# Kernel optimization log

Measured on AMD Instinct MI355X. Metric: run time of the kernel, lower is better.

## Reference

```python
import jax, jax.numpy as jnp
import numpy as np

B, T, C = 8, 512, 2048          # batch streams, qlen, hidden_size
H, Z = 32, 64                   # num_heads, head_size; A = H*Z = attention_hidden_size
A = H * Z
TMX, TDX = 32, 64               # TIME_MIX_EXTRA_DIM, TIME_DECAY_EXTRA_DIM
EPS = 1e-5 * 8.0**2             # ln_x eps = 1e-5 * head_size_divisor**2


def setup_inputs() -> dict:
    key = jax.random.key(0)
    ks = jax.random.split(key, 24)
    def rn(i, shape, scale=1.0):
        return jax.random.normal(ks[i], shape, jnp.float32) * scale
    inv_c = 1.0 / np.sqrt(C)
    return {
        "hidden_states": rn(0, (B * T, C)),
        "positions": jnp.zeros((B * T,), jnp.int32),
        "input_kv_state": jnp.zeros((B, H, Z, Z), jnp.float32),
        "input_shift_state": rn(1, (B, C)),
        "time_maa_x": rn(2, (1, 1, C), 0.1),
        "time_maa_w": rn(3, (1, 1, C), 0.1),
        "time_maa_k": rn(4, (1, 1, C), 0.1),
        "time_maa_v": rn(5, (1, 1, C), 0.1),
        "time_maa_r": rn(6, (1, 1, C), 0.1),
        "time_maa_g": rn(7, (1, 1, C), 0.1),
        "time_maa_w1": rn(8, (C, TMX * 5), inv_c),
        "time_maa_w2": rn(9, (5, TMX, C), 1.0 / np.sqrt(TMX)),
        "time_decay": rn(10, (1, 1, A), 0.5),
        "time_decay_w1": rn(11, (C, TDX), inv_c),
        "time_decay_w2": rn(12, (TDX, A), 0.01),
        "time_faaaa": rn(13, (H, Z), 0.1),
        "W_r": rn(14, (C, A), inv_c),
        "W_k": rn(15, (C, A), inv_c),
        "W_v": rn(16, (C, A), inv_c),
        "W_g": rn(17, (C, A), inv_c),
        "W_o": rn(18, (A, C), inv_c),
        "ln_w": 1.0 + rn(19, (C,), 0.1),
        "ln_b": rn(20, (C,), 0.1),
    }


def _rwkv6_forward(hidden_states, positions, input_kv_state, input_shift_state,
                   time_maa_x, time_maa_w, time_maa_k, time_maa_v, time_maa_r,
                   time_maa_g, time_maa_w1, time_maa_w2, time_decay,
                   time_decay_w1, time_decay_w2, time_faaaa,
                   W_r, W_k, W_v, W_g, W_o, ln_w, ln_b):
    x = hidden_states.reshape(B, T, C)
    pos0_is_zero = positions.reshape(B, T)[:, 0] == 0
    reset = jnp.where(pos0_is_zero, -100.0, 0.0)  # [B]
    # kill shift state for fresh sequences (matches * exp(-100))
    shift = input_shift_state * jnp.exp(reset)[:, None]  # [B, C]

    # token-shift mixing (shift state broadcast over T, as in source)
    xx = shift[:, None, :] - x  # [B, T, C]
    xxx = x + xx * time_maa_x
    mix = jnp.tanh(xxx @ time_maa_w1).reshape(B, T, 5, TMX)
    mix = jnp.einsum('btfe,fec->fbtc', mix, time_maa_w2)  # [5, B, T, C]
    mw, mk, mv, mr, mg = mix

    td_in = x + xx * (time_maa_w + mw)
    kx = x + xx * (time_maa_k + mk)
    vx = x + xx * (time_maa_v + mv)
    rx = x + xx * (time_maa_r + mr)
    gx = x + xx * (time_maa_g + mg)

    r = rx @ W_r
    k = kx @ W_k
    v = vx @ W_v
    g = jax.nn.silu(gx @ W_g)  # [B, T, A]

    w = time_decay + jnp.tanh(td_in @ time_decay_w1) @ time_decay_w2
    w = -jnp.exp(w.astype(jnp.float32))  # log-decay, [B, T, A]

    # split heads -> [T, B, H, Z] for scan
    def to_tbhz(a):
        return a.reshape(B, T, H, Z).transpose(1, 0, 2, 3)
    r_s, k_s, v_s, w_s = to_tbhz(r), to_tbhz(k), to_tbhz(v), to_tbhz(w)
    # zero out carried state at t=0 for fresh sequences
    w_s = w_s.at[0].add(reset[:, None, None])

    u = time_faaaa  # [H, Z]

    def step(S, rkvw):
        # S: [B, H, K, V] (key-dim x value-dim state)
        r_t, k_t, v_t, w_t = rkvw  # each [B, H, Z]
        kv = k_t[..., :, None] * v_t[..., None, :]  # [B, H, K, V]
        o = jnp.einsum('bhk,bhkv->bhv', r_t, S + u[None, :, :, None] * kv)
        S = jnp.exp(w_t)[..., None] * S + kv
        return S, o

    S_out, o = jax.lax.scan(step, input_kv_state, (r_s, k_s, v_s, w_s))
    xo = o.transpose(1, 0, 2, 3).reshape(B * T, C)  # [B*T, C]

    # GroupNorm over heads (num_groups = H)
    xg = xo.reshape(B * T, H, Z)
    mu = xg.mean(-1, keepdims=True)
    var = xg.var(-1, keepdims=True)
    xn = ((xg - mu) * jax.lax.rsqrt(var + EPS)).reshape(B * T, C) * ln_w + ln_b

    out = (xn.reshape(B, T, C) * g) @ W_o  # [B, T, C]
    return out.reshape(B * T, C)


def reference(hidden_states, positions, input_kv_state, input_shift_state,
              time_maa_x, time_maa_w, time_maa_k, time_maa_v, time_maa_r,
              time_maa_g, time_maa_w1, time_maa_w2, time_decay,
              time_decay_w1, time_decay_w2, time_faaaa,
              W_r, W_k, W_v, W_g, W_o, ln_w, ln_b):
    return _rwkv6_forward(hidden_states, positions, input_kv_state,
                          input_shift_state, time_maa_x, time_maa_w,
                          time_maa_k, time_maa_v, time_maa_r, time_maa_g,
                          time_maa_w1, time_maa_w2, time_decay, time_decay_w1,
                          time_decay_w2, time_faaaa, W_r, W_k, W_v, W_g, W_o,
                          ln_w, ln_b)
```

## Files before the change

### kernel.cpp

```cpp
#include <hip/hip_runtime.h>
#include <cmath>

#define NB 8
#define NT 512
#define NC 2048
#define NH 32
#define NZ 64
static constexpr float GN_EPS = 1e-5f * 64.0f;

typedef _Float16 f16;
typedef __attribute__((ext_vector_type(8))) _Float16 f16x8;
typedef __attribute__((ext_vector_type(4))) _Float16 f16x4;
typedef __attribute__((ext_vector_type(4))) float f4;

static __device__ __forceinline__ void gload16(const void* gp, void* lp) {
  __builtin_amdgcn_global_load_lds(
      (const __attribute__((address_space(1))) void*)gp,
      (__attribute__((address_space(3))) void*)lp, 16, 0, 0);
}

__global__ void k_transpose_cast(const float* __restrict__ in, f16* __restrict__ out,
                                 int R, int Cc) {
  __shared__ float tile[32][33];
  int c0 = blockIdx.x * 32, r0 = blockIdx.y * 32;
  int tx = threadIdx.x, ty = threadIdx.y;
#pragma unroll
  for (int i = 0; i < 4; ++i)
    tile[ty + i * 8][tx] = in[(size_t)(r0 + ty + i * 8) * Cc + c0 + tx];
  __syncthreads();
#pragma unroll
  for (int i = 0; i < 4; ++i)
    out[(size_t)(c0 + ty + i * 8) * R + r0 + tx] = (f16)tile[tx][ty + i * 8];
}

__global__ void k_transpose_split(const float* __restrict__ in, f16* __restrict__ ohi,
                                  f16* __restrict__ olo, int R, int Cc) {
  __shared__ float tile[32][33];
  int c0 = blockIdx.x * 32, r0 = blockIdx.y * 32;
  int tx = threadIdx.x, ty = threadIdx.y;
#pragma unroll
  for (int i = 0; i < 4; ++i)
    tile[ty + i * 8][tx] = in[(size_t)(r0 + ty + i * 8) * Cc + c0 + tx];
  __syncthreads();
#pragma unroll
  for (int i = 0; i < 4; ++i) {
    float v = tile[tx][ty + i * 8];
    f16 h = (f16)v;
    size_t o = (size_t)(c0 + ty + i * 8) * R + r0 + tx;
    ohi[o] = h;
    olo[o] = (f16)(v - (float)h);
  }
}

__global__ void k_tsplit_w2(const float* __restrict__ in0, f16* __restrict__ ohi0,
                            f16* __restrict__ olo0) {
  __shared__ float tile[32][33];
  int f = blockIdx.z;
  const float* in = in0 + (size_t)f * 32 * 2048;
  f16* ohi = ohi0 + (size_t)f * 2048 * 32;
  f16* olo = olo0 + (size_t)f * 2048 * 32;
  int c0 = blockIdx.x * 32;
  int tx = threadIdx.x, ty = threadIdx.y;
#pragma unroll
  for (int i = 0; i < 4; ++i)
    tile[ty + i * 8][tx] = in[(size_t)(ty + i * 8) * 2048 + c0 + tx];
  __syncthreads();
#pragma unroll
  for (int i = 0; i < 4; ++i) {
    float v = tile[tx][ty + i * 8];
    f16 h = (f16)v;
    size_t o = (size_t)(c0 + ty + i * 8) * 32 + tx;
    ohi[o] = h;
    olo[o] = (f16)(v - (float)h);
  }
}

__global__ void k_xxx(const float* __restrict__ hs, const float* __restrict__ shift_st,
                      const int* __restrict__ positions, const float* __restrict__ maa_x,
                      float* __restrict__ xxx) {
  int i = blockIdx.x * blockDim.x + threadIdx.x;
  int idx = i * 4;
  int c = idx & (NC - 1);
  int t = idx >> 11;
  int b = t >> 9;
  float er = (positions[b * NT] == 0) ? expf(-100.0f) : 1.0f;
  const float4 x = *(const float4*)(hs + idx);
  const float4 sh = *(const float4*)(shift_st + b * NC + c);
  const float4 mx = *(const float4*)(maa_x + c);
  float4 o;
  o.x = x.x + (sh.x * er - x.x) * mx.x;
  o.y = x.y + (sh.y * er - x.y) * mx.y;
  o.z = x.z + (sh.z * er - x.z) * mx.z;
  o.w = x.w + (sh.w * er - x.w) * mx.w;
  *(float4*)(xxx + idx) = o;
}

static __device__ __forceinline__ void split4(const float4 v, int base, f16x8& hi, f16x8& lo) {
  float x[4] = {v.x, v.y, v.z, v.w};
#pragma unroll
  for (int j = 0; j < 4; ++j) {
    f16 h = (f16)x[j];
    hi[base + j] = h;
    lo[base + j] = (f16)(x[j] - (float)h);
  }
}

__global__ __launch_bounds__(64) void k_mix1_split(const float* __restrict__ A,
                                                   const f16* __restrict__ Bhi,
                                                   const f16* __restrict__ Blo,
                                                   float* __restrict__ out) {
  int m0 = blockIdx.x * 16, n0 = blockIdx.y * 16;
  int lane = threadIdx.x, lr = lane & 15, kq = lane >> 4;
  f4 acc = {0.f, 0.f, 0.f, 0.f};
  const float* ap = A + (size_t)(m0 + lr) * 2048 + kq * 8;
  const f16* bh0 = Bhi + (size_t)(n0 + lr) * 2048 + kq * 8;
  const f16* bl0 = Blo + (size_t)(n0 + lr) * 2048 + kq * 8;
  for (int k0 = 0; k0 < 2048; k0 += 32) {
    f16x8 ah, al;
    split4(*(const float4*)(ap + k0), 0, ah, al);
    split4(*(const float4*)(ap + k0 + 4), 4, ah, al);
    f16x8 bh = *(const f16x8*)(bh0 + k0);
    f16x8 bl = *(const f16x8*)(bl0 + k0);
    acc = __builtin_amdgcn_mfma_f32_16x16x32_f16(ah, bh, acc, 0, 0, 0);
    acc = __builtin_amdgcn_mfma_f32_16x16x32_f16(ah, bl, acc, 0, 0, 0);
    acc = __builtin_amdgcn_mfma_f32_16x16x32_f16(al, bh, acc, 0, 0, 0);
  }
#pragma unroll
  for (int r = 0; r < 4; ++r)
    out[(size_t)(m0 + kq * 4 + r) * 160 + n0 + lr] = tanhf(acc[r]);
}

__global__ __launch_bounds__(64) void k_tmp5_split(const float* __restrict__ mixb,
    const f16* __restrict__ Bhi, const f16* __restrict__ Blo,
    const float* __restrict__ hs, const float* __restrict__ shift_st,
    const int* __restrict__ positions,
    const float* __restrict__ maa_w, const float* __restrict__ maa_k,
    const float* __restrict__ maa_v, const float* __restrict__ maa_r,
    const float* __restrict__ maa_g,
    float* __restrict__ tdin, f16* __restrict__ kx, f16* __restrict__ vx,
    f16* __restrict__ rx, f16* __restrict__ gx) {
  int m0 = blockIdx.x * 16, n0 = blockIdx.y * 16;
  int lane = threadIdx.x, lr = lane & 15, kq = lane >> 4;
  f4 acc[5];
#pragma unroll
  for (int f = 0; f < 5; ++f) acc[f] = (f4){0.f, 0.f, 0.f, 0.f};
  const float* ap = mixb + (size_t)(m0 + lr) * 160 + kq * 8;
#pragma unroll
  for (int f = 0; f < 5; ++f) {
    f16x8 ah, al;
    split4(*(const float4*)(ap + f * 32), 0, ah, al);
    split4(*(const float4*)(ap + f * 32 + 4), 4, ah, al);
    size_t bi = ((size_t)f * 2048 + n0 + lr) * 32 + kq * 8;
    f16x8 bh = *(const f16x8*)(Bhi + bi);
    f16x8 bl = *(const f16x8*)(Blo + bi);
    acc[f] = __builtin_amdgcn_mfma_f32_16x16x32_f16(ah, bh, acc[f], 0, 0, 0);
    acc[f] = __builtin_amdgcn_mfma_f32_16x16x32_f16(ah, bl, acc[f], 0, 0, 0);
    acc[f] = __builtin_amdgcn_mfma_f32_16x16x32_f16(al, bh, acc[f], 0, 0, 0);
  }
  int c = n0 + lr;
  float mw = maa_w[c], mk = maa_k[c], mv = maa_v[c], mr = maa_r[c], mg = maa_g[c];
#pragma unroll
  for (int r = 0; r < 4; ++r) {
    int t = m0 + kq * 4 + r;
    int b = t >> 9;
    float er = (positions[b * NT] == 0) ? expf(-100.0f) : 1.0f;
    float x = hs[(size_t)t * NC + c];
    float xxv = shift_st[b * NC + c] * er - x;
    size_t oi = (size_t)t * NC + c;
    tdin[oi] = x + xxv * (mw + acc[0][r]);
    kx[oi] = (f16)(x + xxv * (mk + acc[1][r]));
    vx[oi] = (f16)(x + xxv * (mv + acc[2][r]));
    rx[oi] = (f16)(x + xxv * (mr + acc[3][r]));
    gx[oi] = (f16)(x + xxv * (mg + acc[4][r]));
  }
}

__global__ __launch_bounds__(64) void k_wd1_split(const float* __restrict__ A,
                                                  const f16* __restrict__ Bhi,
                                                  const f16* __restrict__ Blo,
                                                  float* __restrict__ out) {
  int m0 = blockIdx.x * 16, n0 = blockIdx.y * 16;
  int lane = threadIdx.x, lr = lane & 15, kq = lane >> 4;
  f4 acc = {0.f, 0.f, 0.f, 0.f};
  const float* ap = A + (size_t)(m0 + lr) * 2048 + kq * 8;
  const f16* bh0 = Bhi + (size_t)(n0 + lr) * 2048 + kq * 8;
  const f16* bl0 = Blo + (size_t)(n0 + lr) * 2048 + kq * 8;
  for (int k0 = 0; k0 < 2048; k0 += 32) {
    f16x8 ah, al;
    split4(*(const float4*)(ap + k0), 0, ah, al);
    split4(*(const float4*)(ap + k0 + 4), 4, ah, al);
    f16x8 bh = *(const f16x8*)(bh0 + k0);
    f16x8 bl = *(const f16x8*)(bl0 + k0);
    acc = __builtin_amdgcn_mfma_f32_16x16x32_f16(ah, bh, acc, 0, 0, 0);
    acc = __builtin_amdgcn_mfma_f32_16x16x32_f16(ah, bl, acc, 0, 0, 0);
    acc = __builtin_amdgcn_mfma_f32_16x16x32_f16(al, bh, acc, 0, 0, 0);
  }
#pragma unroll
  for (int r = 0; r < 4; ++r)
    out[(size_t)(m0 + kq * 4 + r) * 64 + n0 + lr] = tanhf(acc[r]);
}

__global__ __launch_bounds__(64) void k_wdecay_split(const float* __restrict__ A,
                                                     const f16* __restrict__ Bhi,
                                                     const f16* __restrict__ Blo,
                                                     const float* __restrict__ time_decay,
                                                     float* __restrict__ wout) {
  int m0 = blockIdx.x * 16, n0 = blockIdx.y * 16;
  int lane = threadIdx.x, lr = lane & 15, kq = lane >> 4;
  f4 acc = {0.f, 0.f, 0.f, 0.f};
#pragma unroll
  for (int kk = 0; kk < 2; ++kk) {
    f16x8 ah, al;
    const float* ap = A + (size_t)(m0 + lr) * 64 + kk * 32 + kq * 8;
    split4(*(const float4*)ap, 0, ah, al);
    split4(*(const float4*)(ap + 4), 4, ah, al);
    size_t bi = (size_t)(n0 + lr) * 64 + kk * 32 + kq * 8;
    f16x8 bh = *(const f16x8*)(Bhi + bi);
    f16x8 bl = *(const f16x8*)(Blo + bi);
    acc = __builtin_amdgcn_mfma_f32_16x16x32_f16(ah, bh, acc, 0, 0, 0);
    acc = __builtin_amdgcn_mfma_f32_16x16x32_f16(ah, bl, acc, 0, 0, 0);
    acc = __builtin_amdgcn_mfma_f32_16x16x32_f16(al, bh, acc, 0, 0, 0);
  }
  int c = n0 + lr;
  float td = time_decay[c];
#pragma unroll
  for (int r = 0; r < 4; ++r) {
    int t = m0 + kq * 4 + r;
    wout[(size_t)t * NC + c] = -expf(td + acc[r]);
  }
}

#define GBM 128
#define GBN 128
#define GBK 64

template <int EPI>
__global__ __launch_bounds__(256) void k_gemm_big(const f16* __restrict__ A,
                                                  const f16* __restrict__ Bt,
                                                  float* __restrict__ Cf,
                                                  f16* __restrict__ Cb, int K) {
  __shared__ __align__(16) f16 As[2][GBM][GBK];
  __shared__ __align__(16) f16 Bs[2][GBN][GBK];
  int nwg = gridDim.x * gridDim.y;
  int wg = blockIdx.y * gridDim.x + blockIdx.x;
  int swz = (wg & 7) * (nwg >> 3) + (wg >> 3);
  int n0 = (swz % gridDim.x) * GBN;
  int m0 = (swz / gridDim.x) * GBM;
  int tid = threadIdx.x;
  int wid = tid >> 6, lane = tid & 63;
  int wr = wid >> 1, wc = wid & 1;
  int lr = lane & 15, kq = lane >> 4;
  int sw = lr & 7;
  int gunit = (lane & 7) ^ (lane >> 3);
  const f16* aL = A + (size_t)(m0 + wid * 32 + (lane >> 3)) * K + gunit * 8;
  const f16* bL = Bt + (size_t)(n0 + wid * 32 + (lane >> 3)) * K + gunit * 8;
  f4 acc[4][4];
#pragma unroll
  for (int m = 0; m < 4; ++m)
#pragma unroll
    for (int n = 0; n < 4; ++n) acc[m][n] = (f4){0.f, 0.f, 0.f, 0.f};

  auto stage = [&](int buf, int t) {
    int k0 = t * GBK;
#pragma unroll
    for (int i = 0; i < 4; ++i) {
      gload16(aL + k0 + (size_t)i * 8 * K, &As[buf][wid * 32 + i * 8][0]);
      gload16(bL + k0 + (size_t)i * 8 * K, &Bs[buf][wid * 32 + i * 8][0]);
    }
  };

  int niter = K / GBK;
  stage(0, 0);
  stage(1, 1);
  for (int it = 0; it < niter; ++it) {
    if (it == niter - 1)
      asm volatile("s_waitcnt vmcnt(0)" ::: "memory");
    else
      asm volatile("s_waitcnt vmcnt(8)" ::: "memory");
    __builtin_amdgcn_sched_barrier(0);
    __builtin_amdgcn_s_barrier();
    int cur = it & 1;
#pragma unroll
    for (int kk = 0; kk < 2; ++kk) {
      f16x8 af[4], bfv[4];
      int un = ((kk * 4 + kq) ^ sw) * 8;
#pragma unroll
      for (int m = 0; m < 4; ++m)
        af[m] = *(const f16x8*)&As[cur][wr * 64 + m * 16 + lr][un];
#pragma unroll
      for (int n = 0; n < 4; ++n)
        bfv[n] = *(const f16x8*)&Bs[cur][wc * 64 + n * 16 + lr][un];
#pragma unroll
      for (int m = 0; m < 4; ++m)
#pragma unroll
        for (int n = 0; n < 4; ++n)
          acc[m][n] = __builtin_amdgcn_mfma_f32_16x16x32_f16(af[m], bfv[n], acc[m][n], 0, 0, 0);
    }
    __builtin_amdgcn_s_barrier();
    if (it + 2 < niter) stage(cur, it + 2);
  }
#pragma unroll
  for (int m = 0; m < 4; ++m) {
    int row0 = m0 + wr * 64 + m * 16 + kq * 4;
#pragma unroll
    for (int n = 0; n < 4; ++n) {
      int col = n0 + wc * 64 + n * 16 + lr;
#pragma unroll
      for (int r = 0; r < 4; ++r) {
        float v = acc[m][n][r];
        size_t oi = (size_t)(row0 + r) * NC + col;
        if (EPI == 0) {
          Cf[oi] = v;
        } else {
          float s = v / (1.0f + expf(-v));
          Cb[oi] = (f16)s;
        }
      }
    }
  }
}

__global__ __launch_bounds__(64) void k_scanB(
    const float* rb, const float* __restrict__ kb,
    const float* __restrict__ vb, const float* __restrict__ wb,
    const float* __restrict__ kvstate, const int* __restrict__ positions,
    const float* __restrict__ faaaa, f16* __restrict__ o,
    float* rtil, float* __restrict__ Ebuf, float* __restrict__ Dbuf) {
  int blk = blockIdx.x;
  int bh = blk >> 3, c = blk & 7;
  int b = bh >> 5, h = bh & 31;
  int zz = threadIdx.x;
  __shared__ __align__(16) float shR[64];
  __shared__ __align__(16) float shE[64];
  __shared__ __align__(16) float shK[64];
  float S[64];
  if (c == 0) {
    const float* S0 = kvstate + (size_t)bh * 4096;
#pragma unroll
    for (int j = 0; j < 64; ++j) S[j] = S0[j * 64 + zz];
  } else {
#pragma unroll
    for (int j = 0; j < 64; ++j) S[j] = 0.f;
  }
  float u = faaaa[h * 64 + zz];
  float reset = (positions[b * NT] == 0) ? -100.0f : 0.0f;
  const size_t base = ((size_t)(b * NT) + c * 64) * NC + h * 64 + zz;
  float vr = rb[base], vk = kb[base], vw = wb[base], vv = vb[base];
  float Pw = 1.0f;
  for (int t = 0; t < 64; ++t) {
    float nr = 0.f, nk = 0.f, nw = 0.f, nv = 0.f;
    if (t + 1 < 64) {
      size_t idx = base + (size_t)(t + 1) * NC;
      nr = rb[idx]; nk = kb[idx]; nw = wb[idx]; nv = vb[idx];
    }
    float ww = vw;
    if (c == 0 && t == 0) ww += reset;
    float ew = expf(ww);
    shR[zz] = vr; shE[zz] = ew; shK[zz] = vk;
    float q = vr * u * vk;
    q += __shfl_xor(q, 1);  q += __shfl_xor(q, 2);  q += __shfl_xor(q, 4);
    q += __shfl_xor(q, 8);  q += __shfl_xor(q, 16); q += __shfl_xor(q, 32);
    __syncthreads();
    if (c > 0) rtil[base + (size_t)t * NC] = vr * Pw;
    Pw *= ew;
    float oacc = vv * q;
#pragma unroll
    for (int k0 = 0; k0 < 64; k0 += 4) {
      f4 r4 = *(const f4*)&shR[k0];
      f4 e4 = *(const f4*)&shE[k0];
      f4 k4 = *(const f4*)&shK[k0];
#pragma unroll
      for (int j = 0; j < 4; ++j) {
        oacc = fmaf(r4[j], S[k0 + j], oacc);
        S[k0 + j] = fmaf(e4[j], S[k0 + j], k4[j] * vv);
      }
    }
    o[base + (size_t)t * NC] = (f16)oacc;
    __syncthreads();
    vr = nr; vk = nk; vw = nw; vv = nv;
  }
  if (c < 7) {
    float* E = Ebuf + ((size_t)bh * 7 + c) * 4096;
#pragma unroll
    for (int j = 0; j < 64; ++j) E[j * 64 + zz] = S[j];
  }
  Dbuf[((size_t)bh * 8 + c) * 64 + zz] = Pw;
}

__global__ __launch_bounds__(256) void k_comb(float* __restrict__ Ebuf,
                                              const float* __restrict__ Dbuf) {
  int bh = blockIdx.x, tid = threadIdx.x;
  int k = tid >> 2, v0 = (tid & 3) * 16;
  float* base = Ebuf + (size_t)bh * 7 * 4096;
  float S[16];
#pragma unroll
  for (int j = 0; j < 16; ++j) S[j] = base[k * 64 + v0 + j];
  for (int c = 2; c <= 7; ++c) {
    float d = Dbuf[((size_t)bh * 8 + (c - 1)) * 64 + k];
    float* slot = base + (size_t)(c - 1) * 4096;
#pragma unroll
    for (int j = 0; j < 16; ++j) {
      S[j] = fmaf(d, S[j], slot[k * 64 + v0 + j]);
      slot[k * 64 + v0 + j] = S[j];
    }
  }
}

__global__ __launch_bounds__(256) void k_fix(const float* __restrict__ rtil,
                                             const float* __restrict__ Ebuf,
                                             f16* __restrict__ o) {
  int blk = blockIdx.x;
  int bh = blk / 7, cm = blk - bh * 7;
  int c = cm + 1;
  int b = bh >> 5, h = bh & 31;
  __shared__ float Rs[64][65];
  __shared__ float Ss[64][65];
  int tid = threadIdx.x;
  const float* rsrc = rtil + ((size_t)(b * NT) + c * 64) * NC + h * NZ;
  const float* ssrc = Ebuf + ((size_t)bh * 7 + cm) * 4096;
#pragma unroll
  for (int q = 0; q < 4; ++q) {
    int li = tid * 4 + q;
    int rr = li >> 4, cc = (li & 15) * 4;
    float4 x = *(const float4*)(rsrc + (size_t)rr * NC + cc);
    Rs[rr][cc] = x.x; Rs[rr][cc + 1] = x.y; Rs[rr][cc + 2] = x.z; Rs[rr][cc + 3] = x.w;
    float4 y = *(const float4*)(ssrc + rr * 64 + cc);
    Ss[rr][cc] = y.x; Ss[rr][cc + 1] = y.y; Ss[rr][cc + 2] = y.z; Ss[rr][cc + 3] = y.w;
  }
  __syncthreads();
  int t = tid >> 2, v0 = (tid & 3) * 16;
  float acc[16];
#pragma unroll
  for (int j = 0; j < 16; ++j) acc[j] = 0.f;
  for (int k = 0; k < 64; ++k) {
    float rv = Rs[t][k];
#pragma unroll
    for (int j = 0; j < 16; ++j) acc[j] = fmaf(rv, Ss[k][v0 + j], acc[j]);
  }
  f16* op = o + ((size_t)(b * NT) + c * 64 + t) * NC + h * NZ + v0;
  f16x8 o0 = *(f16x8*)op, o1 = *(f16x8*)(op + 8);
#pragma unroll
  for (int j = 0; j < 8; ++j) {
    o0[j] = (f16)((float)o0[j] + acc[j]);
    o1[j] = (f16)((float)o1[j] + acc[j + 8]);
  }
  *(f16x8*)op = o0;
  *(f16x8*)(op + 8) = o1;
}

__global__ __launch_bounds__(256) void k_gnorm(const f16* __restrict__ xo, const f16* __restrict__ g,
    const float* __restrict__ ln_w, const float* __restrict__ ln_b, f16* __restrict__ y) {
  int t = blockIdx.x;
  int tid = threadIdx.x;
  int c = tid * 8;
  f16x8 xv8 = *(const f16x8*)(xo + (size_t)t * NC + c);
  float xv[8];
#pragma unroll
  for (int j = 0; j < 8; ++j) xv[j] = (float)xv8[j];
  float s = 0.f, ss = 0.f;
#pragma unroll
  for (int j = 0; j < 8; ++j) { s += xv[j]; ss += xv[j] * xv[j]; }
  s += __shfl_xor(s, 1); ss += __shfl_xor(ss, 1);
  s += __shfl_xor(s, 2); ss += __shfl_xor(ss, 2);
  s += __shfl_xor(s, 4); ss += __shfl_xor(ss, 4);
  float mu = s * (1.0f / 64.0f);
  float var = ss * (1.0f / 64.0f) - mu * mu;
  float rstd = rsqrtf(var + GN_EPS);
  f16x8 gv = *(const f16x8*)(g + (size_t)t * NC + c);
  f16x8 ov;
#pragma unroll
  for (int j = 0; j < 8; ++j) {
    float xn = (xv[j] - mu) * rstd * ln_w[c + j] + ln_b[c + j];
    ov[j] = (f16)(xn * (float)gv[j]);
  }
  *(f16x8*)(y + (size_t)t * NC + c) = ov;
}

extern "C" void kernel_launch(void* const* d_in, const int* in_sizes, int n_in,
                              void* d_out, int out_size, void* d_ws, size_t ws_size,
                              hipStream_t stream) {
  const float* hs = (const float*)d_in[0];
  const int* positions = (const int*)d_in[1];
  const float* kvstate = (const float*)d_in[2];
  const float* shift_st = (const float*)d_in[3];
  const float* maa_x = (const float*)d_in[4];
  const float* maa_w = (const float*)d_in[5];
  const float* maa_k = (const float*)d_in[6];
  const float* maa_v = (const float*)d_in[7];
  const float* maa_r = (const float*)d_in[8];
  const float* maa_g = (const float*)d_in[9];
  const float* maa_w1 = (const float*)d_in[10];
  const float* maa_w2 = (const float*)d_in[11];
  const float* time_decay = (const float*)d_in[12];
  const float* decay_w1 = (const float*)d_in[13];
  const float* decay_w2 = (const float*)d_in[14];
  const float* faaaa = (const float*)d_in[15];
  const float* W_r = (const float*)d_in[16];
  const float* W_k = (const float*)d_in[17];
  const float* W_v = (const float*)d_in[18];
  const float* W_g = (const float*)d_in[19];
  const float* W_o = (const float*)d_in[20];
  const float* ln_w = (const float*)d_in[21];
  const float* ln_b = (const float*)d_in[22];

  char* ws = (char*)d_ws;
  size_t off = 0;
  auto alloc = [&](size_t n) {
    char* p = ws + off;
    off += (n + 255) & ~(size_t)255;
    return p;
  };
  f16* w1t_hi = (f16*)alloc(160ull * 2048 * 2);
  f16* w1t_lo = (f16*)alloc(160ull * 2048 * 2);
  f16* w2t_hi = (f16*)alloc(5ull * 2048 * 32 * 2);
  f16* w2t_lo = (f16*)alloc(5ull * 2048 * 32 * 2);
  f16* dw1t_hi = (f16*)alloc(64ull * 2048 * 2);
  f16* dw1t_lo = (f16*)alloc(64ull * 2048 * 2);
  f16* dw2t_hi = (f16*)alloc(2048ull * 64 * 2);
  f16* dw2t_lo = (f16*)alloc(2048ull * 64 * 2);
  float* mixb = (float*)alloc(4096ull * 160 * 4);
  float* wd1 = (float*)alloc(4096ull * 64 * 4);
  char* R_A = alloc(4096ull * 2048 * 4);
  char* R_B = alloc(4096ull * 2048 * 4);
  char* R_C = alloc(4096ull * 2048 * 4);
  char* R_D = alloc(4096ull * 2048 * 4);
  char* R_E = alloc(4096ull * 2048 * 2);
  char* F12 = alloc(4096ull * 2048 * 4);
  char* F3 = alloc(4096ull * 2048 * 2);
  char* F4 = alloc(4096ull * 2048 * 2);

  float* xxx = (float*)R_A;
  float* tdin = (float*)R_A;
  float* wbuf = (float*)R_A;
  float* rbuf = (float*)R_B;
  float* kbuf = (float*)R_C;
  float* vbuf = (float*)R_D;
  f16* wstage = (f16*)R_E;
  f16* obuf = (f16*)R_E;
  f16* kx = (f16*)F12;
  f16* vx = (f16*)(F12 + 4096ull * 2048 * 2);
  float* Ebuf = (float*)F12;
  float* Dbuf = (float*)(F12 + 29360128);
  f16* rx = (f16*)F3;
  f16* gbuf = (f16*)F3;
  f16* gx = (f16*)F4;
  f16* wt_o = (f16*)F4;

  dim3 tb(32, 8);
  k_transpose_split<<<dim3(5, 64), tb, 0, stream>>>(maa_w1, w1t_hi, w1t_lo, 2048, 160);
  k_tsplit_w2<<<dim3(64, 1, 5), tb, 0, stream>>>(maa_w2, w2t_hi, w2t_lo);
  k_transpose_split<<<dim3(2, 64), tb, 0, stream>>>(decay_w1, dw1t_hi, dw1t_lo, 2048, 64);
  k_transpose_split<<<dim3(64, 2), tb, 0, stream>>>(decay_w2, dw2t_hi, dw2t_lo, 64, 2048);

  k_xxx<<<8192, 256, 0, stream>>>(hs, shift_st, positions, maa_x, xxx);
  k_mix1_split<<<dim3(256, 10), 64, 0, stream>>>(xxx, w1t_hi, w1t_lo, mixb);
  k_tmp5_split<<<dim3(256, 128), 64, 0, stream>>>(mixb, w2t_hi, w2t_lo, hs, shift_st,
      positions, maa_w, maa_k, maa_v, maa_r, maa_g, tdin, kx, vx, rx, gx);
  k_wd1_split<<<dim3(256, 4), 64, 0, stream>>>(tdin, dw1t_hi, dw1t_lo, wd1);
  k_wdecay_split<<<dim3(256, 128), 64, 0, stream>>>(wd1, dw2t_hi, dw2t_lo, time_decay, wbuf);

  dim3 gg(2048 / GBN, 4096 / GBM);
  k_transpose_cast<<<dim3(64, 64), tb, 0, stream>>>(W_r, wstage, 2048, 2048);
  k_gemm_big<0><<<gg, 256, 0, stream>>>(rx, wstage, rbuf, nullptr, 2048);
  k_transpose_cast<<<dim3(64, 64), tb, 0, stream>>>(W_k, wstage, 2048, 2048);
  k_gemm_big<0><<<gg, 256, 0, stream>>>(kx, wstage, kbuf, nullptr, 2048);
  k_transpose_cast<<<dim3(64, 64), tb, 0, stream>>>(W_v, wstage, 2048, 2048);
  k_gemm_big<0><<<gg, 256, 0, stream>>>(vx, wstage, vbuf, nullptr, 2048);
  k_transpose_cast<<<dim3(64, 64), tb, 0, stream>>>(W_g, wstage, 2048, 2048);
  k_gemm_big<2><<<gg, 256, 0, stream>>>(gx, wstage, nullptr, gbuf, 2048);
  k_transpose_cast<<<dim3(64, 64), tb, 0, stream>>>(W_o, wt_o, 2048, 2048);

  k_scanB<<<2048, 64, 0, stream>>>(rbuf, kbuf, vbuf, wbuf, kvstate, positions, faaaa,
                                   obuf, rbuf, Ebuf, Dbuf);
  k_comb<<<256, 256, 0, stream>>>(Ebuf, Dbuf);
  k_fix<<<1792, 256, 0, stream>>>(rbuf, Ebuf, obuf);

  k_gnorm<<<4096, 256, 0, stream>>>(obuf, gbuf, ln_w, ln_b, obuf);
  k_gemm_big<0><<<gg, 256, 0, stream>>>(obuf, wt_o, (float*)d_out, nullptr, 2048);
}
```

Baseline: 639.9 us.

## Double-buffer scan inputs into LDS with async loads in four-step groups

The chunked WKV scan now stages r, k, w and v rows for four timesteps at a time into LDS. It uses global_load_lds with a double buffer and explicit vmcnt waits, replacing per-timestep register prefetch and three barrier-guarded shared arrays. Decay exponentials are computed for all four steps at once, which cuts barriers from two per timestep to two per group. The goal is to hide global-load latency in a latency-bound scan. The cost is more LDS, and correctness depends on hand-written waitcnt logic and on the single-wave block running in lockstep.

After: 640.2 us. No clear change (+0.1%).

```diff
diff --git a/kernel.cpp b/kernel.cpp
--- a/kernel.cpp
+++ b/kernel.cpp
@@ -320,7 +320,7 @@
   }
 }
 
-__global__ __launch_bounds__(64) void k_scanB(
+__global__ __launch_bounds__(64) void k_scanD(
     const float* rb, const float* __restrict__ kb,
     const float* __restrict__ vb, const float* __restrict__ wb,
     const float* __restrict__ kvstate, const int* __restrict__ positions,
@@ -330,9 +330,8 @@
   int bh = blk >> 3, c = blk & 7;
   int b = bh >> 5, h = bh & 31;
   int zz = threadIdx.x;
-  __shared__ __align__(16) float shR[64];
-  __shared__ __align__(16) float shE[64];
-  __shared__ __align__(16) float shK[64];
+  __shared__ __align__(16) float stg[2][4][4][64];
+  __shared__ __align__(16) float shE[4][64];
   float S[64];
   if (c == 0) {
     const float* S0 = kvstate + (size_t)bh * 4096;
@@ -344,40 +343,63 @@
   }
   float u = faaaa[h * 64 + zz];
   float reset = (positions[b * NT] == 0) ? -100.0f : 0.0f;
-  const size_t base = ((size_t)(b * NT) + c * 64) * NC + h * 64 + zz;
-  float vr = rb[base], vk = kb[base], vw = wb[base], vv = vb[base];
+  const int row0 = b * NT + c * 64;
+  const int lrow = zz >> 4, lcol = (zz & 15) * 4;
+
+  auto stage = [&](int buf, int T) {
+    size_t goff = (size_t)(row0 + T + lrow) * NC + h * 64 + lcol;
+    gload16(rb + goff, &stg[buf][0][0][0]);
+    gload16(kb + goff, &stg[buf][1][0][0]);
+    gload16(wb + goff, &stg[buf][2][0][0]);
+    gload16(vb + goff, &stg[buf][3][0][0]);
+  };
+  stage(0, 0);
+  stage(1, 4);
   float Pw = 1.0f;
-  for (int t = 0; t < 64; ++t) {
-    float nr = 0.f, nk = 0.f, nw = 0.f, nv = 0.f;
-    if (t + 1 < 64) {
-      size_t idx = base + (size_t)(t + 1) * NC;
-      nr = rb[idx]; nk = kb[idx]; nw = wb[idx]; nv = vb[idx];
+  for (int g = 0; g < 16; ++g) {
+    if (g == 15)
+      asm volatile("s_waitcnt vmcnt(0)" ::: "memory");
+    else
+      asm volatile("s_waitcnt vmcnt(4)" ::: "memory");
+    __builtin_amdgcn_sched_barrier(0);
+    __syncthreads();
+    int cur = g & 1;
+    float ew[4];
+#pragma unroll
+    for (int j = 0; j < 4; ++j) {
+      float ww = stg[cur][2][j][zz];
+      if (c == 0 && g == 0 && j == 0) ww += reset;
+      ew[j] = expf(ww);
+      shE[j][zz] = ew[j];
     }
-    float ww = vw;
-    if (c == 0 && t == 0) ww += reset;
-    float ew = expf(ww);
-    shR[zz] = vr; shE[zz] = ew; shK[zz] = vk;
-    float q = vr * u * vk;
-    q += __shfl_xor(q, 1);  q += __shfl_xor(q, 2);  q += __shfl_xor(q, 4);
-    q += __shfl_xor(q, 8);  q += __shfl_xor(q, 16); q += __shfl_xor(q, 32);
     __syncthreads();
-    if (c > 0) rtil[base + (size_t)t * NC] = vr * Pw;
-    Pw *= ew;
-    float oacc = vv * q;
-#pragma unroll
-    for (int k0 = 0; k0 < 64; k0 += 4) {
-      f4 r4 = *(const f4*)&shR[k0];
-      f4 e4 = *(const f4*)&shE[k0];
-      f4 k4 = *(const f4*)&shK[k0];
-#pragma unroll
-      for (int j = 0; j < 4; ++j) {
-        oacc = fmaf(r4[j], S[k0 + j], oacc);
-        S[k0 + j] = fmaf(e4[j], S[k0 + j], k4[j] * vv);
+#pragma unroll
+    for (int j = 0; j < 4; ++j) {
+      int t = g * 4 + j;
+      size_t rowoff = (size_t)(row0 + t) * NC + h * 64;
+      float vr = stg[cur][0][j][zz];
+      float vk = stg[cur][1][j][zz];
+      float vv = stg[cur][3][j][zz];
+      float q = vr * u * vk;
+      q += __shfl_xor(q, 1);  q += __shfl_xor(q, 2);  q += __shfl_xor(q, 4);
+      q += __shfl_xor(q, 8);  q += __shfl_xor(q, 16); q += __shfl_xor(q, 32);
+      if (c > 0) rtil[rowoff + zz] = vr * Pw;
+      Pw *= ew[j];
+      float oacc = vv * q;
+#pragma unroll
+      for (int k0 = 0; k0 < 64; k0 += 4) {
+        f4 r4 = *(const f4*)&stg[cur][0][j][k0];
+        f4 e4 = *(const f4*)&shE[j][k0];
+        f4 k4 = *(const f4*)&stg[cur][1][j][k0];
+#pragma unroll
+        for (int jj = 0; jj < 4; ++jj) {
+          oacc = fmaf(r4[jj], S[k0 + jj], oacc);
+          S[k0 + jj] = fmaf(e4[jj], S[k0 + jj], k4[jj] * vv);
+        }
       }
+      o[rowoff + zz] = (f16)oacc;
     }
-    o[base + (size_t)t * NC] = (f16)oacc;
-    __syncthreads();
-    vr = nr; vk = nk; vw = nw; vv = nv;
+    if (g + 2 < 16) stage(cur, (g + 2) * 4);
   }
   if (c < 7) {
     float* E = Ebuf + ((size_t)bh * 7 + c) * 4096;
@@ -570,7 +592,7 @@
   k_gemm_big<2><<<gg, 256, 0, stream>>>(gx, wstage, nullptr, gbuf, 2048);
   k_transpose_cast<<<dim3(64, 64), tb, 0, stream>>>(W_o, wt_o, 2048, 2048);
 
-  k_scanB<<<2048, 64, 0, stream>>>(rbuf, kbuf, vbuf, wbuf, kvstate, positions, faaaa,
+  k_scanD<<<2048, 64, 0, stream>>>(rbuf, kbuf, vbuf, wbuf, kvstate, positions, faaaa,
                                    obuf, rbuf, Ebuf, Dbuf);
   k_comb<<<256, 256, 0, stream>>>(Ebuf, Dbuf);
   k_fix<<<1792, 256, 0, stream>>>(rbuf, Ebuf, obuf);
```
